# Kernel tuning notes

Measured on AMD Instinct MI355X. Metric: run time of the kernel, lower is better.

The kernel has to match this reference:

```python
import jax, jax.numpy as jnp
import numpy as np

B, T, D, H, L = 256, 128, 32, 512, 6
EPS = 1e-5


def setup_inputs() -> dict:
    key = jax.random.key(0)
    ks = jax.random.split(key, 12)
    sc = 0.02
    rn = lambda k, shp, s: (jax.random.normal(k, shp, jnp.float32) * s)
    return {
        "x": rn(ks[0], (B, T, D), 1.0),
        "w_proj": rn(ks[1], (H, D), sc),
        "b_proj": jnp.zeros((H,), jnp.float32),
        "w_ih": rn(ks[2], (L, 4 * H, H), sc),
        "w_hh": rn(ks[3], (L, 4 * H, H), sc),
        "b_ih": jnp.zeros((L, 4 * H), jnp.float32),
        "b_hh": jnp.zeros((L, 4 * H), jnp.float32),
        "ln_g": jnp.ones((L, H), jnp.float32),
        "ln_b": jnp.zeros((L, H), jnp.float32),
        "w1": rn(ks[4], (H, H), sc),
        "b1": jnp.zeros((H,), jnp.float32),
        "w2": rn(ks[5], (H // 2, H), sc),
        "b2": jnp.zeros((H // 2,), jnp.float32),
        "w3": rn(ks[6], (1, H // 2), sc),
        "b3": jnp.zeros((1,), jnp.float32),
    }


def _layer_norm(x, g, b):
    mu = jnp.mean(x, axis=-1, keepdims=True)
    var = jnp.mean(jnp.square(x - mu), axis=-1, keepdims=True)
    return (x - mu) * jax.lax.rsqrt(var + EPS) * g + b


def _lstm_layer(x, wih, whh, bih, bhh):
    # Precompute input-gate contributions for the whole sequence: [B,T,4H]
    xg = jnp.einsum("bth,gh->btg", x, wih) + (bih + bhh)
    h0 = jnp.zeros((x.shape[0], whh.shape[1]), x.dtype)

    def step(carry, xg_t):
        h, c = carry
        gates = xg_t + h @ whh.T  # [B,4H], torch gate order i,f,g,o
        i, f, g, o = jnp.split(gates, 4, axis=-1)
        i = jax.nn.sigmoid(i)
        f = jax.nn.sigmoid(f)
        g = jnp.tanh(g)
        o = jax.nn.sigmoid(o)
        c = f * c + i * g
        h = o * jnp.tanh(c)
        return (h, c), h

    _, hs = jax.lax.scan(step, (h0, h0), jnp.swapaxes(xg, 0, 1))  # hs: [T,B,H]
    return jnp.swapaxes(hs, 0, 1)  # [B,T,H]


def reference(x, w_proj, b_proj, w_ih, w_hh, b_ih, b_hh, ln_g, ln_b,
              w1, b1, w2, b2, w3, b3):
    h_prev = x @ w_proj.T + b_proj  # input projection: [B,T,H]
    for i in range(L):
        out = _lstm_layer(h_prev, w_ih[i], w_hh[i], b_ih[i], b_hh[i])
        out = _layer_norm(out, ln_g[i], ln_b[i])
        # dropout is identity in eval mode
        if i > 0:
            out = out + h_prev
        h_prev = out
    last = out[:, -1, :]  # [B,H]
    z = jax.nn.relu(last @ w1.T + b1)
    z = jax.nn.relu(z @ w2.T + b2)
    return z @ w3.T + b3  # [B,1]
```

## Files before the change

kernel.cpp:

```cpp
#include <hip/hip_runtime.h>
#include <hip/hip_bf16.h>
#include <stdint.h>

#define BB 256
#define TT 128
#define DD 32
#define HH 512
#define NL 6

typedef __attribute__((ext_vector_type(8))) short short8;
typedef __attribute__((ext_vector_type(4))) float f32x4;

__device__ __forceinline__ unsigned short f2bf(float f) {
    union { float f; unsigned u; } v; v.f = f;
    unsigned r = v.u + 0x7fff + ((v.u >> 16) & 1);
    return (unsigned short)(r >> 16);
}
__device__ __forceinline__ float bf2f(unsigned short s) {
    union { unsigned u; float f; } v; v.u = ((unsigned)s) << 16;
    return v.f;
}
__device__ __forceinline__ float fsig(float x) { return 1.0f / (1.0f + __expf(-x)); }
__device__ __forceinline__ float ftanh(float x) {
    float e = __expf(-2.0f * fabsf(x));
    float t = (1.0f - e) / (1.0f + e);
    return x < 0.0f ? -t : t;
}

__device__ __forceinline__ size_t xt_off(int slot, int ks, int kg, int row) {
    return ((((size_t)slot * 16 + ks) * 4 + kg) * 256 + row) * 8;
}

__device__ __forceinline__ int4 g_load16_cc(const void* p) {
    int4 r;
    asm volatile("global_load_dwordx4 %0, %1, off sc0 sc1" : "=v"(r) : "v"(p) : "memory");
    return r;
}
__device__ __forceinline__ void g_store16_cc(void* p, int4 v) {
    union { int4 q; unsigned long long d[2]; } u; u.q = v;
    void* p2 = (void*)((char*)p + 8);
    asm volatile("global_store_dwordx2 %0, %1, off sc0 sc1" :: "v"(p), "v"(u.d[0]) : "memory");
    asm volatile("global_store_dwordx2 %0, %1, off sc0 sc1" :: "v"(p2), "v"(u.d[1]) : "memory");
}

__device__ __forceinline__ void poll_ge(unsigned int* p, unsigned target) {
    int guard = 0;
    while (__hip_atomic_load(p, __ATOMIC_RELAXED, __HIP_MEMORY_SCOPE_AGENT) < target &&
           ++guard < (1 << 17)) {}
}

__global__ __launch_bounds__(256) void k_zero(unsigned int* __restrict__ p, int n) {
    int i = blockIdx.x * 256 + threadIdx.x;
    if (i < n) p[i] = 0;
}

__global__ __launch_bounds__(256) void k_convert(const float* __restrict__ wih, const float* __restrict__ whh,
                                                 unsigned short* __restrict__ wih_bf, unsigned short* __restrict__ whh_bf,
                                                 int n4) {
    int i = blockIdx.x * 256 + threadIdx.x;
    if (i >= n4) return;
    float4 a = ((const float4*)wih)[i];
    float4 b = ((const float4*)whh)[i];
    ushort4 ra; ra.x = f2bf(a.x); ra.y = f2bf(a.y); ra.z = f2bf(a.z); ra.w = f2bf(a.w);
    ushort4 rb; rb.x = f2bf(b.x); rb.y = f2bf(b.y); rb.z = f2bf(b.z); rb.w = f2bf(b.w);
    ((ushort4*)wih_bf)[i] = ra;
    ((ushort4*)whh_bf)[i] = rb;
}

__global__ __launch_bounds__(512) void k_proj(const float* __restrict__ x, const float* __restrict__ wp,
                                              const float* __restrict__ bp,
                                              unsigned short* __restrict__ abfT) {
    __shared__ float xs[64][DD];
    int m0 = blockIdx.x * 64;
    for (int i = threadIdx.x; i < 64 * DD; i += 512)
        xs[i >> 5][i & 31] = x[(size_t)(m0 + (i >> 5)) * DD + (i & 31)];
    __syncthreads();
    int n = threadIdx.x;
    float w[DD];
#pragma unroll
    for (int k = 0; k < DD; k++) w[k] = wp[n * DD + k];
    float bias = bp[n];
    const int ks = n >> 5, kg = (n >> 3) & 3, e = n & 7;
    for (int r = 0; r < 64; r++) {
        float acc = bias;
#pragma unroll
        for (int k = 0; k < DD; k++) acc += xs[r][k] * w[k];
        int flat = m0 + r;
        int b = flat >> 7, t = flat & 127;
        abfT[xt_off(t, ks, kg, b) + e] = f2bf(acc);
    }
}

__device__ __forceinline__ void do_ln(int l, int tln, int row, int li, bool final_out,
                                      const unsigned short* __restrict__ hbuf,
                                      unsigned short* __restrict__ xring,
                                      const float* __restrict__ ln_g, const float* __restrict__ ln_b,
                                      float* __restrict__ xfinal) {
    const int ks = li >> 1, kgb = (li & 1) * 2;
    int4 h0 = g_load16_cc(hbuf + xt_off(l * 2 + (tln & 1), ks, kgb, row));
    int4 h1 = g_load16_cc(hbuf + xt_off(l * 2 + (tln & 1), ks, kgb + 1, row));
    int4 r0, r1;
    const bool res = (l > 0);
    if (res) {
        int slot = (l - 1) * 16 + (tln & 15);
        r0 = g_load16_cc(xring + xt_off(slot, ks, kgb, row));
        r1 = g_load16_cc(xring + xt_off(slot, ks, kgb + 1, row));
    }
    asm volatile("s_waitcnt vmcnt(0)" ::: "memory");
    __builtin_amdgcn_sched_barrier(0);
    const unsigned short* hu0 = (const unsigned short*)&h0;
    const unsigned short* hu1 = (const unsigned short*)&h1;
    float v[16];
    float s = 0.f, ss = 0.f;
#pragma unroll
    for (int e = 0; e < 8; e++) { v[e] = bf2f(hu0[e]); v[e + 8] = bf2f(hu1[e]); }
#pragma unroll
    for (int e = 0; e < 16; e++) { s += v[e]; ss += v[e] * v[e]; }
#pragma unroll
    for (int off = 1; off < 32; off <<= 1) {
        s += __shfl_xor(s, off);
        ss += __shfl_xor(ss, off);
    }
    float mu = s * (1.f / 512.f);
    float var = ss * (1.f / 512.f) - mu * mu;
    float rs = rsqrtf(var + 1e-5f);
    const unsigned short* ru0 = (const unsigned short*)&r0;
    const unsigned short* ru1 = (const unsigned short*)&r1;
    float y[16];
#pragma unroll
    for (int e = 0; e < 16; e++) {
        float yy = (v[e] - mu) * rs * ln_g[l * 512 + li * 16 + e] + ln_b[l * 512 + li * 16 + e];
        if (res) yy += bf2f(e < 8 ? ru0[e] : ru1[e - 8]);
        y[e] = yy;
    }
    if (final_out) {
        float* dst = xfinal + (size_t)row * 512 + li * 16;
#pragma unroll
        for (int q = 0; q < 4; q++)
            *(float4*)(dst + q * 4) = (float4){y[q * 4], y[q * 4 + 1], y[q * 4 + 2], y[q * 4 + 3]};
    } else {
        unsigned short ys[16];
#pragma unroll
        for (int e = 0; e < 16; e++) ys[e] = f2bf(y[e]);
        int slot = l * 16 + (tln & 15);
        g_store16_cc(xring + xt_off(slot, ks, kgb, row), *(int4*)&ys[0]);
        g_store16_cc(xring + xt_off(slot, ks, kgb + 1, row), *(int4*)&ys[8]);
    }
}

__global__ __launch_bounds__(256, 1) void k_mega(
    const unsigned short* __restrict__ wih_bf,
    const unsigned short* __restrict__ whh_bf,
    const unsigned short* __restrict__ a_bfT,
    const float* __restrict__ bih_all, const float* __restrict__ bhh_all,
    const float* __restrict__ ln_g, const float* __restrict__ ln_b,
    unsigned short* __restrict__ xring,
    unsigned short* __restrict__ hbuf,
    float* __restrict__ xfinal,
    unsigned int* __restrict__ cnt)
{
    __shared__ unsigned short smem[128 * 512];
    __shared__ unsigned short hstage[128 * 34];

    const int blk = blockIdx.x;
    const int l = blk >> 5;
    const int rr_ = blk & 31;
    const int g = rr_ >> 4;
    const int ui = rr_ & 15;
    const int tid = threadIdx.x, lane = tid & 63, w = tid >> 6;
    const int u0 = ui * 32;
    const int gb0 = g * 128;
    const int wb0 = gb0 + w * 32;
    const int uu = lane & 15;
    const int kg = lane >> 4;

    const unsigned short* wih = wih_bf + (size_t)l * 2048 * 512;
    const unsigned short* whh = whh_bf + (size_t)l * 2048 * 512;
    unsigned int* c1  = cnt + (l * 2 + g) * 64;
    unsigned int* c1n = cnt + ((l + 1) * 2 + g) * 64;
    unsigned int* c2  = cnt + (12 + l * 2 + g) * 64;
    unsigned int* c2u = cnt + (12 + (l - 1) * 2 + g) * 64;

    for (int c = tid; c < 128 * 64; c += 256) {
        int rr = c >> 6, k16 = c & 63;
        int grow = (rr >> 5) * 512 + u0 + ((rr >> 4) & 1) * 16 + (rr & 15);
        int4 v = *(const int4*)(whh + (size_t)grow * 512 + k16 * 8);
        int baddr = (rr * 1024 + k16 * 16) ^ ((rr & 7) << 4);
        *(int4*)((char*)smem + baddr) = v;
    }
    __syncthreads();

    float biasg[8];
#pragma unroll
    for (int rt = 0; rt < 8; rt++) {
        int grow = (rt >> 1) * 512 + u0 + ((rt & 1) << 4) + uu;
        biasg[rt] = bih_all[l * 2048 + grow] + bhh_all[l * 2048 + grow];
    }

    const int ln_row = gb0 + ui * 8 + w * 2 + (lane >> 5);
    const int li = lane & 31;
    f32x4 cst[4];
#pragma unroll
    for (int q = 0; q < 4; q++) cst[q] = (f32x4){0.f, 0.f, 0.f, 0.f};

#pragma unroll 1
    for (int t = 0; t < TT; ++t) {
        if (tid == 0) {
            if (t > 0) poll_ge(c1, 16u * (unsigned)t);
            if (l < 5 && t >= 17) poll_ge(c1n, 16u * (unsigned)(t - 15));
        }
        __syncthreads();

        if (t > 0 && l < 5) {
            do_ln(l, t - 1, ln_row, li, false, hbuf, xring, ln_g, ln_b, xfinal);
            asm volatile("s_waitcnt vmcnt(0)" ::: "memory");
            __syncthreads();
            if (tid == 0)
                __hip_atomic_fetch_add(c2, 1u, __ATOMIC_RELAXED, __HIP_MEMORY_SCOPE_AGENT);
        }

        if (l > 0) {
            if (tid == 0) poll_ge(c2u, 16u * (unsigned)(t + 1));
            __syncthreads();
        }

        f32x4 acc[2][8];
#pragma unroll
        for (int bt = 0; bt < 2; bt++)
#pragma unroll
            for (int rt = 0; rt < 8; rt++)
                acc[bt][rt] = (f32x4){biasg[rt], biasg[rt], biasg[rt], biasg[rt]};

#pragma unroll
        for (int half = 0; half < 2; half++) {
            short8 ax[2][8];
            if (l == 0) {
#pragma unroll
                for (int bt = 0; bt < 2; bt++)
#pragma unroll
                    for (int k8 = 0; k8 < 8; k8++)
                        ax[bt][k8] = *(const short8*)(a_bfT + xt_off(t, half * 8 + k8, kg, wb0 + bt * 16 + uu));
            } else {
                int slot = (l - 1) * 16 + (t & 15);
                int4 ai[2][8];
#pragma unroll
                for (int bt = 0; bt < 2; bt++)
#pragma unroll
                    for (int k8 = 0; k8 < 8; k8++)
                        ai[bt][k8] = g_load16_cc(xring + xt_off(slot, half * 8 + k8, kg, wb0 + bt * 16 + uu));
                asm volatile("s_waitcnt vmcnt(0)" ::: "memory");
                __builtin_amdgcn_sched_barrier(0);
#pragma unroll
                for (int bt = 0; bt < 2; bt++)
#pragma unroll
                    for (int k8 = 0; k8 < 8; k8++)
                        ax[bt][k8] = *(short8*)&ai[bt][k8];
            }
#pragma unroll
            for (int k8 = 0; k8 < 8; k8++) {
                int ks = half * 8 + k8;
#pragma unroll
                for (int rt = 0; rt < 8; rt++) {
                    short8 bfr = *(const short8*)(wih + (size_t)((rt >> 1) * 512 + u0 + ((rt & 1) << 4) + uu) * 512 +
                                                  ks * 32 + kg * 8);
                    acc[0][rt] = __builtin_amdgcn_mfma_f32_16x16x32_bf16(ax[0][k8], bfr, acc[0][rt], 0, 0, 0);
                    acc[1][rt] = __builtin_amdgcn_mfma_f32_16x16x32_bf16(ax[1][k8], bfr, acc[1][rt], 0, 0, 0);
                }
            }
        }

        if (t > 0) {
            const int hslot = l * 2 + ((t - 1) & 1);
#pragma unroll
            for (int half = 0; half < 2; half++) {
                int4 ai[2][8];
#pragma unroll
                for (int bt = 0; bt < 2; bt++)
#pragma unroll
                    for (int k8 = 0; k8 < 8; k8++)
                        ai[bt][k8] = g_load16_cc(hbuf + xt_off(hslot, half * 8 + k8, kg, wb0 + bt * 16 + uu));
                asm volatile("s_waitcnt vmcnt(0)" ::: "memory");
                __builtin_amdgcn_sched_barrier(0);
#pragma unroll
                for (int k8 = 0; k8 < 8; k8++) {
                    int k2 = ((half * 8 + k8) * 32 + kg * 8) * 2;
                    short8 ah0 = *(short8*)&ai[0][k8];
                    short8 ah1 = *(short8*)&ai[1][k8];
#pragma unroll
                    for (int rt = 0; rt < 8; rt++) {
                        int rr = rt * 16 + uu;
                        int baddr = (rr * 1024 + k2) ^ ((rr & 7) << 4);
                        short8 bh = *(const short8*)((const char*)smem + baddr);
                        acc[0][rt] = __builtin_amdgcn_mfma_f32_16x16x32_bf16(ah0, bh, acc[0][rt], 0, 0, 0);
                        acc[1][rt] = __builtin_amdgcn_mfma_f32_16x16x32_bf16(ah1, bh, acc[1][rt], 0, 0, 0);
                    }
                }
            }
        }

#pragma unroll
        for (int bt = 0; bt < 2; bt++)
#pragma unroll
            for (int usub = 0; usub < 2; usub++) {
                f32x4 iq = acc[bt][0 + usub], fq = acc[bt][2 + usub];
                f32x4 gq = acc[bt][4 + usub], oq = acc[bt][6 + usub];
#pragma unroll
                for (int j = 0; j < 4; j++) {
                    float i_ = fsig(iq[j]);
                    float f_ = fsig(fq[j]);
                    float g_ = ftanh(gq[j]);
                    float o_ = fsig(oq[j]);
                    float c = f_ * cst[bt * 2 + usub][j] + i_ * g_;
                    cst[bt * 2 + usub][j] = c;
                    float h = o_ * ftanh(c);
                    hstage[(w * 32 + bt * 16 + kg * 4 + j) * 34 + usub * 16 + uu] = f2bf(h);
                }
            }
        __syncthreads();
        {
            const int hdst = l * 2 + (t & 1);
#pragma unroll
            for (int c = 0; c < 2; c++) {
                int idx = c * 256 + tid;
                int kgp = idx >> 7, rowp = idx & 127;
                int4 v = *(const int4*)(hstage + rowp * 34 + kgp * 8);
                g_store16_cc(hbuf + xt_off(hdst, ui, kgp, gb0 + rowp), v);
            }
        }
        asm volatile("s_waitcnt vmcnt(0)" ::: "memory");
        __syncthreads();
        if (tid == 0)
            __hip_atomic_fetch_add(c1, 1u, __ATOMIC_RELAXED, __HIP_MEMORY_SCOPE_AGENT);
    }

    if (tid == 0) poll_ge(c1, 16u * 128u);
    __syncthreads();
    if (l < 5) {
        do_ln(l, TT - 1, ln_row, li, false, hbuf, xring, ln_g, ln_b, xfinal);
        asm volatile("s_waitcnt vmcnt(0)" ::: "memory");
        __syncthreads();
        if (tid == 0)
            __hip_atomic_fetch_add(c2, 1u, __ATOMIC_RELAXED, __HIP_MEMORY_SCOPE_AGENT);
    } else {
        do_ln(l, TT - 1, ln_row, li, true, hbuf, xring, ln_g, ln_b, xfinal);
    }
}

__global__ __launch_bounds__(512) void k_mlp1(const float* __restrict__ xfinal, const float* __restrict__ w1,
                                              const float* __restrict__ b1, float* __restrict__ z1) {
    __shared__ float xs[512];
    int b = blockIdx.x;
    xs[threadIdx.x] = xfinal[(size_t)b * 512 + threadIdx.x];
    __syncthreads();
    int n = threadIdx.x;
    const float4* wr = (const float4*)(w1 + (size_t)n * 512);
    float acc = b1[n];
#pragma unroll 4
    for (int k4 = 0; k4 < 128; k4++) {
        float4 wv = wr[k4];
        acc += xs[k4 * 4 + 0] * wv.x + xs[k4 * 4 + 1] * wv.y + xs[k4 * 4 + 2] * wv.z + xs[k4 * 4 + 3] * wv.w;
    }
    z1[(size_t)b * 512 + n] = fmaxf(acc, 0.f);
}

__global__ __launch_bounds__(256) void k_mlp2(const float* __restrict__ z1, const float* __restrict__ w2,
                                              const float* __restrict__ b2, float* __restrict__ z2) {
    __shared__ float xs[512];
    int b = blockIdx.x;
    xs[threadIdx.x] = z1[(size_t)b * 512 + threadIdx.x];
    xs[threadIdx.x + 256] = z1[(size_t)b * 512 + threadIdx.x + 256];
    __syncthreads();
    int n = threadIdx.x;
    const float4* wr = (const float4*)(w2 + (size_t)n * 512);
    float acc = b2[n];
#pragma unroll 4
    for (int k4 = 0; k4 < 128; k4++) {
        float4 wv = wr[k4];
        acc += xs[k4 * 4 + 0] * wv.x + xs[k4 * 4 + 1] * wv.y + xs[k4 * 4 + 2] * wv.z + xs[k4 * 4 + 3] * wv.w;
    }
    z2[(size_t)b * 256 + n] = fmaxf(acc, 0.f);
}

__global__ __launch_bounds__(256) void k_mlp3(const float* __restrict__ z2, const float* __restrict__ w3,
                                              const float* __restrict__ b3, float* __restrict__ outp) {
    __shared__ float red[4];
    int b = blockIdx.x;
    int tid = threadIdx.x;
    float p = z2[(size_t)b * 256 + tid] * w3[tid];
#pragma unroll
    for (int off = 32; off > 0; off >>= 1) p += __shfl_down(p, off);
    if ((tid & 63) == 0) red[tid >> 6] = p;
    __syncthreads();
    if (tid == 0) outp[b] = red[0] + red[1] + red[2] + red[3] + b3[0];
}

extern "C" void kernel_launch(void* const* d_in, const int* in_sizes, int n_in,
                              void* d_out, int out_size, void* d_ws, size_t ws_size,
                              hipStream_t stream) {
    const float* x      = (const float*)d_in[0];
    const float* w_proj = (const float*)d_in[1];
    const float* b_proj = (const float*)d_in[2];
    const float* w_ih   = (const float*)d_in[3];
    const float* w_hh   = (const float*)d_in[4];
    const float* b_ih   = (const float*)d_in[5];
    const float* b_hh   = (const float*)d_in[6];
    const float* ln_g   = (const float*)d_in[7];
    const float* ln_b   = (const float*)d_in[8];
    const float* w1 = (const float*)d_in[9];  const float* b1 = (const float*)d_in[10];
    const float* w2 = (const float*)d_in[11]; const float* b2 = (const float*)d_in[12];
    const float* w3 = (const float*)d_in[13]; const float* b3 = (const float*)d_in[14];
    float* outp = (float*)d_out;

    char* ws = (char*)d_ws;
    size_t off = 0;
    auto alloc = [&](size_t sz) { char* p = ws + off; off += (sz + 255) & ~(size_t)255; return p; };
    unsigned short* a_bfT  = (unsigned short*)alloc((size_t)128 * 131072 * 2);
    unsigned short* wih_bf = (unsigned short*)alloc((size_t)NL * 2048 * 512 * 2);
    unsigned short* whh_bf = (unsigned short*)alloc((size_t)NL * 2048 * 512 * 2);
    unsigned short* xring  = (unsigned short*)alloc((size_t)80 * 131072 * 2);
    unsigned short* hbuf   = (unsigned short*)alloc((size_t)12 * 131072 * 2);
    float*          xfinal = (float*)alloc((size_t)256 * 512 * 4);
    float*          z1     = (float*)alloc((size_t)256 * 512 * 4);
    float*          z2     = (float*)alloc((size_t)256 * 256 * 4);
    unsigned int*   cnt    = (unsigned int*)alloc(2048 * 4);

    k_zero<<<8, 256, 0, stream>>>(cnt, 2048);
    k_convert<<<6144, 256, 0, stream>>>(w_ih, w_hh, wih_bf, whh_bf, (NL * 2048 * 512) / 4);
    k_proj<<<512, 512, 0, stream>>>(x, w_proj, b_proj, a_bfT);

    k_mega<<<192, 256, 0, stream>>>(wih_bf, whh_bf, a_bfT, b_ih, b_hh, ln_g, ln_b,
                                    xring, hbuf, xfinal, cnt);

    k_mlp1<<<256, 512, 0, stream>>>(xfinal, w1, b1, z1);
    k_mlp2<<<256, 256, 0, stream>>>(z1, w2, b2, z2);
    k_mlp3<<<256, 256, 0, stream>>>(z2, w3, b3, outp);
}
```

Measured before the change: 9.014 ms.

## Deepen h/x ring buffers and use cached loads instead of coherent bypass loads

```diff
diff --git a/kernel.cpp b/kernel.cpp
--- a/kernel.cpp
+++ b/kernel.cpp
@@ -31,11 +31,6 @@
     return ((((size_t)slot * 16 + ks) * 4 + kg) * 256 + row) * 8;
 }
 
-__device__ __forceinline__ int4 g_load16_cc(const void* p) {
-    int4 r;
-    asm volatile("global_load_dwordx4 %0, %1, off sc0 sc1" : "=v"(r) : "v"(p) : "memory");
-    return r;
-}
 __device__ __forceinline__ void g_store16_cc(void* p, int4 v) {
     union { int4 q; unsigned long long d[2]; } u; u.q = v;
     void* p2 = (void*)((char*)p + 8);
@@ -95,25 +90,25 @@
                                       const unsigned short* __restrict__ hbuf,
                                       unsigned short* __restrict__ xring,
                                       const float* __restrict__ ln_g, const float* __restrict__ ln_b,
-                                      float* __restrict__ xfinal) {
+                                      float* __restrict__ xfinal, int D_h, int D_x) {
     const int ks = li >> 1, kgb = (li & 1) * 2;
-    int4 h0 = g_load16_cc(hbuf + xt_off(l * 2 + (tln & 1), ks, kgb, row));
-    int4 h1 = g_load16_cc(hbuf + xt_off(l * 2 + (tln & 1), ks, kgb + 1, row));
-    int4 r0, r1;
+    const int hslot = l * D_h + (tln & (D_h - 1));
+    short8 h0 = *(const short8*)(hbuf + xt_off(hslot, ks, kgb, row));
+    short8 h1 = *(const short8*)(hbuf + xt_off(hslot, ks, kgb + 1, row));
+    short8 r0 = h0, r1 = h1;
     const bool res = (l > 0);
     if (res) {
-        int slot = (l - 1) * 16 + (tln & 15);
-        r0 = g_load16_cc(xring + xt_off(slot, ks, kgb, row));
-        r1 = g_load16_cc(xring + xt_off(slot, ks, kgb + 1, row));
-    }
-    asm volatile("s_waitcnt vmcnt(0)" ::: "memory");
-    __builtin_amdgcn_sched_barrier(0);
-    const unsigned short* hu0 = (const unsigned short*)&h0;
-    const unsigned short* hu1 = (const unsigned short*)&h1;
+        int slot = (l - 1) * D_x + (tln & (D_x - 1));
+        r0 = *(const short8*)(xring + xt_off(slot, ks, kgb, row));
+        r1 = *(const short8*)(xring + xt_off(slot, ks, kgb + 1, row));
+    }
     float v[16];
     float s = 0.f, ss = 0.f;
 #pragma unroll
-    for (int e = 0; e < 8; e++) { v[e] = bf2f(hu0[e]); v[e + 8] = bf2f(hu1[e]); }
+    for (int e = 0; e < 8; e++) {
+        v[e] = bf2f((unsigned short)h0[e]);
+        v[e + 8] = bf2f((unsigned short)h1[e]);
+    }
 #pragma unroll
     for (int e = 0; e < 16; e++) { s += v[e]; ss += v[e] * v[e]; }
 #pragma unroll
@@ -124,25 +119,25 @@
     float mu = s * (1.f / 512.f);
     float var = ss * (1.f / 512.f) - mu * mu;
     float rs = rsqrtf(var + 1e-5f);
-    const unsigned short* ru0 = (const unsigned short*)&r0;
-    const unsigned short* ru1 = (const unsigned short*)&r1;
     float y[16];
 #pragma unroll
     for (int e = 0; e < 16; e++) {
         float yy = (v[e] - mu) * rs * ln_g[l * 512 + li * 16 + e] + ln_b[l * 512 + li * 16 + e];
-        if (res) yy += bf2f(e < 8 ? ru0[e] : ru1[e - 8]);
+        if (res) yy += bf2f((unsigned short)(e < 8 ? r0[e] : r1[e - 8]));
         y[e] = yy;
     }
     if (final_out) {
         float* dst = xfinal + (size_t)row * 512 + li * 16;
 #pragma unroll
-        for (int q = 0; q < 4; q++)
-            *(float4*)(dst + q * 4) = (float4){y[q * 4], y[q * 4 + 1], y[q * 4 + 2], y[q * 4 + 3]};
+        for (int q = 0; q < 4; q++) {
+            float4 t4 = (float4){y[q * 4], y[q * 4 + 1], y[q * 4 + 2], y[q * 4 + 3]};
+            g_store16_cc(dst + q * 4, *(int4*)&t4);
+        }
     } else {
         unsigned short ys[16];
 #pragma unroll
         for (int e = 0; e < 16; e++) ys[e] = f2bf(y[e]);
-        int slot = l * 16 + (tln & 15);
+        int slot = l * D_x + (tln & (D_x - 1));
         g_store16_cc(xring + xt_off(slot, ks, kgb, row), *(int4*)&ys[0]);
         g_store16_cc(xring + xt_off(slot, ks, kgb + 1, row), *(int4*)&ys[8]);
     }
@@ -157,16 +152,17 @@
     unsigned short* __restrict__ xring,
     unsigned short* __restrict__ hbuf,
     float* __restrict__ xfinal,
-    unsigned int* __restrict__ cnt)
+    unsigned int* __restrict__ cnt,
+    int D_h, int D_x)
 {
     __shared__ unsigned short smem[128 * 512];
     __shared__ unsigned short hstage[128 * 34];
 
     const int blk = blockIdx.x;
-    const int l = blk >> 5;
-    const int rr_ = blk & 31;
-    const int g = rr_ >> 4;
-    const int ui = rr_ & 15;
+    const int j = (blk & 7) * 24 + (blk >> 3);
+    const int l = j >> 5;
+    const int g = (j >> 4) & 1;
+    const int ui = j & 15;
     const int tid = threadIdx.x, lane = tid & 63, w = tid >> 6;
     const int u0 = ui * 32;
     const int gb0 = g * 128;
@@ -206,13 +202,17 @@
 #pragma unroll 1
     for (int t = 0; t < TT; ++t) {
         if (tid == 0) {
-            if (t > 0) poll_ge(c1, 16u * (unsigned)t);
-            if (l < 5 && t >= 17) poll_ge(c1n, 16u * (unsigned)(t - 15));
+            if (t > 0) {
+                poll_ge(c1, 16u * (unsigned)t);
+                if (t - 1 >= D_h)
+                    (void)__hip_atomic_load(c1, __ATOMIC_ACQUIRE, __HIP_MEMORY_SCOPE_AGENT);
+            }
+            if (l < 5 && t >= D_x + 1) poll_ge(c1n, 16u * (unsigned)(t - D_x + 1));
         }
         __syncthreads();
 
         if (t > 0 && l < 5) {
-            do_ln(l, t - 1, ln_row, li, false, hbuf, xring, ln_g, ln_b, xfinal);
+            do_ln(l, t - 1, ln_row, li, false, hbuf, xring, ln_g, ln_b, xfinal, D_h, D_x);
             asm volatile("s_waitcnt vmcnt(0)" ::: "memory");
             __syncthreads();
             if (tid == 0)
@@ -220,7 +220,11 @@
         }
 
         if (l > 0) {
-            if (tid == 0) poll_ge(c2u, 16u * (unsigned)(t + 1));
+            if (tid == 0) {
+                poll_ge(c2u, 16u * (unsigned)(t + 1));
+                if (t >= D_x)
+                    (void)__hip_atomic_load(c2u, __ATOMIC_ACQUIRE, __HIP_MEMORY_SCOPE_AGENT);
+            }
             __syncthreads();
         }
 
@@ -231,31 +235,18 @@
             for (int rt = 0; rt < 8; rt++)
                 acc[bt][rt] = (f32x4){biasg[rt], biasg[rt], biasg[rt], biasg[rt]};
 
+        const unsigned short* xsrc = (l == 0)
+            ? (a_bfT + xt_off(t, 0, 0, 0))
+            : (xring + xt_off((l - 1) * D_x + (t & (D_x - 1)), 0, 0, 0));
+
 #pragma unroll
         for (int half = 0; half < 2; half++) {
             short8 ax[2][8];
-            if (l == 0) {
-#pragma unroll
-                for (int bt = 0; bt < 2; bt++)
-#pragma unroll
-                    for (int k8 = 0; k8 < 8; k8++)
-                        ax[bt][k8] = *(const short8*)(a_bfT + xt_off(t, half * 8 + k8, kg, wb0 + bt * 16 + uu));
-            } else {
-                int slot = (l - 1) * 16 + (t & 15);
-                int4 ai[2][8];
-#pragma unroll
-                for (int bt = 0; bt < 2; bt++)
-#pragma unroll
-                    for (int k8 = 0; k8 < 8; k8++)
-                        ai[bt][k8] = g_load16_cc(xring + xt_off(slot, half * 8 + k8, kg, wb0 + bt * 16 + uu));
-                asm volatile("s_waitcnt vmcnt(0)" ::: "memory");
-                __builtin_amdgcn_sched_barrier(0);
-#pragma unroll
-                for (int bt = 0; bt < 2; bt++)
-#pragma unroll
-                    for (int k8 = 0; k8 < 8; k8++)
-                        ax[bt][k8] = *(short8*)&ai[bt][k8];
-            }
+#pragma unroll
+            for (int bt = 0; bt < 2; bt++)
+#pragma unroll
+                for (int k8 = 0; k8 < 8; k8++)
+                    ax[bt][k8] = *(const short8*)(xsrc + xt_off(0, half * 8 + k8, kg, wb0 + bt * 16 + uu));
 #pragma unroll
             for (int k8 = 0; k8 < 8; k8++) {
                 int ks = half * 8 + k8;
@@ -270,29 +261,25 @@
         }
 
         if (t > 0) {
-            const int hslot = l * 2 + ((t - 1) & 1);
+            const unsigned short* hsrc = hbuf + xt_off(l * D_h + ((t - 1) & (D_h - 1)), 0, 0, 0);
 #pragma unroll
             for (int half = 0; half < 2; half++) {
-                int4 ai[2][8];
+                short8 ah[2][8];
 #pragma unroll
                 for (int bt = 0; bt < 2; bt++)
 #pragma unroll
                     for (int k8 = 0; k8 < 8; k8++)
-                        ai[bt][k8] = g_load16_cc(hbuf + xt_off(hslot, half * 8 + k8, kg, wb0 + bt * 16 + uu));
-                asm volatile("s_waitcnt vmcnt(0)" ::: "memory");
-                __builtin_amdgcn_sched_barrier(0);
+                        ah[bt][k8] = *(const short8*)(hsrc + xt_off(0, half * 8 + k8, kg, wb0 + bt * 16 + uu));
 #pragma unroll
                 for (int k8 = 0; k8 < 8; k8++) {
                     int k2 = ((half * 8 + k8) * 32 + kg * 8) * 2;
-                    short8 ah0 = *(short8*)&ai[0][k8];
-                    short8 ah1 = *(short8*)&ai[1][k8];
 #pragma unroll
                     for (int rt = 0; rt < 8; rt++) {
                         int rr = rt * 16 + uu;
                         int baddr = (rr * 1024 + k2) ^ ((rr & 7) << 4);
                         short8 bh = *(const short8*)((const char*)smem + baddr);
-                        acc[0][rt] = __builtin_amdgcn_mfma_f32_16x16x32_bf16(ah0, bh, acc[0][rt], 0, 0, 0);
-                        acc[1][rt] = __builtin_amdgcn_mfma_f32_16x16x32_bf16(ah1, bh, acc[1][rt], 0, 0, 0);
+                        acc[0][rt] = __builtin_amdgcn_mfma_f32_16x16x32_bf16(ah[0][k8], bh, acc[0][rt], 0, 0, 0);
+                        acc[1][rt] = __builtin_amdgcn_mfma_f32_16x16x32_bf16(ah[1][k8], bh, acc[1][rt], 0, 0, 0);
                     }
                 }
             }
@@ -305,20 +292,20 @@
                 f32x4 iq = acc[bt][0 + usub], fq = acc[bt][2 + usub];
                 f32x4 gq = acc[bt][4 + usub], oq = acc[bt][6 + usub];
 #pragma unroll
-                for (int j = 0; j < 4; j++) {
-                    float i_ = fsig(iq[j]);
-                    float f_ = fsig(fq[j]);
-                    float g_ = ftanh(gq[j]);
-                    float o_ = fsig(oq[j]);
-                    float c = f_ * cst[bt * 2 + usub][j] + i_ * g_;
-                    cst[bt * 2 + usub][j] = c;
+                for (int jj = 0; jj < 4; jj++) {
+                    float i_ = fsig(iq[jj]);
+                    float f_ = fsig(fq[jj]);
+                    float g_ = ftanh(gq[jj]);
+                    float o_ = fsig(oq[jj]);
+                    float c = f_ * cst[bt * 2 + usub][jj] + i_ * g_;
+                    cst[bt * 2 + usub][jj] = c;
                     float h = o_ * ftanh(c);
-                    hstage[(w * 32 + bt * 16 + kg * 4 + j) * 34 + usub * 16 + uu] = f2bf(h);
+                    hstage[(w * 32 + bt * 16 + kg * 4 + jj) * 34 + usub * 16 + uu] = f2bf(h);
                 }
             }
         __syncthreads();
         {
-            const int hdst = l * 2 + (t & 1);
+            const int hdst = l * D_h + (t & (D_h - 1));
 #pragma unroll
             for (int c = 0; c < 2; c++) {
                 int idx = c * 256 + tid;
@@ -333,16 +320,20 @@
             __hip_atomic_fetch_add(c1, 1u, __ATOMIC_RELAXED, __HIP_MEMORY_SCOPE_AGENT);
     }
 
-    if (tid == 0) poll_ge(c1, 16u * 128u);
+    if (tid == 0) {
+        poll_ge(c1, 16u * 128u);
+        if (TT - 1 >= D_h)
+            (void)__hip_atomic_load(c1, __ATOMIC_ACQUIRE, __HIP_MEMORY_SCOPE_AGENT);
+    }
     __syncthreads();
     if (l < 5) {
-        do_ln(l, TT - 1, ln_row, li, false, hbuf, xring, ln_g, ln_b, xfinal);
+        do_ln(l, TT - 1, ln_row, li, false, hbuf, xring, ln_g, ln_b, xfinal, D_h, D_x);
         asm volatile("s_waitcnt vmcnt(0)" ::: "memory");
         __syncthreads();
         if (tid == 0)
             __hip_atomic_fetch_add(c2, 1u, __ATOMIC_RELAXED, __HIP_MEMORY_SCOPE_AGENT);
     } else {
-        do_ln(l, TT - 1, ln_row, li, true, hbuf, xring, ln_g, ln_b, xfinal);
+        do_ln(l, TT - 1, ln_row, li, true, hbuf, xring, ln_g, ln_b, xfinal, D_h, D_x);
     }
 }
 
@@ -411,14 +402,28 @@
     const float* w3 = (const float*)d_in[13]; const float* b3 = (const float*)d_in[14];
     float* outp = (float*)d_out;
 
+    const size_t base = (size_t)128 * 131072 * 2
+                      + (size_t)NL * 2048 * 512 * 2
+                      + (size_t)NL * 2048 * 512 * 2
+                      + (size_t)256 * 512 * 4
+                      + (size_t)256 * 512 * 4
+                      + (size_t)256 * 256 * 4
+                      + 2048 * 4
+                      + 16 * 256;
+    int D = 8;
+    for (int cand = 128; cand >= 8; cand >>= 1) {
+        size_t need = base + (size_t)(NL + NL - 1) * cand * 131072 * 2;
+        if (need <= ws_size) { D = cand; break; }
+    }
+
     char* ws = (char*)d_ws;
     size_t off = 0;
     auto alloc = [&](size_t sz) { char* p = ws + off; off += (sz + 255) & ~(size_t)255; return p; };
     unsigned short* a_bfT  = (unsigned short*)alloc((size_t)128 * 131072 * 2);
     unsigned short* wih_bf = (unsigned short*)alloc((size_t)NL * 2048 * 512 * 2);
     unsigned short* whh_bf = (unsigned short*)alloc((size_t)NL * 2048 * 512 * 2);
-    unsigned short* xring  = (unsigned short*)alloc((size_t)80 * 131072 * 2);
-    unsigned short* hbuf   = (unsigned short*)alloc((size_t)12 * 131072 * 2);
+    unsigned short* xring  = (unsigned short*)alloc((size_t)(NL - 1) * D * 131072 * 2);
+    unsigned short* hbuf   = (unsigned short*)alloc((size_t)NL * D * 131072 * 2);
     float*          xfinal = (float*)alloc((size_t)256 * 512 * 4);
     float*          z1     = (float*)alloc((size_t)256 * 512 * 4);
     float*          z2     = (float*)alloc((size_t)256 * 256 * 4);
@@ -429,7 +434,7 @@
     k_proj<<<512, 512, 0, stream>>>(x, w_proj, b_proj, a_bfT);
 
     k_mega<<<192, 256, 0, stream>>>(wih_bf, whh_bf, a_bfT, b_ih, b_hh, ln_g, ln_b,
-                                    xring, hbuf, xfinal, cnt);
+                                    xring, hbuf, xfinal, cnt, D, D);
 
     k_mlp1<<<256, 512, 0, stream>>>(xfinal, w1, b1, z1);
     k_mlp2<<<256, 256, 0, stream>>>(z1, w2, b2, z2);
```

Result: slower. 9.549 ms (+5.9%).
